# Kernel tuning notes

Hardware: AMD Instinct MI355X
Metric: run time of the kernel (lower is better)

## Reference

```python
import jax, jax.numpy as jnp
import numpy as np

DIM_Q = 512
DIM_K = 512
DIM_V = 512
NUM_HEADS = 8
EPS = 1e-5


def _layer_norm(x, g, b):
    m = jnp.mean(x, axis=-1, keepdims=True)
    v = jnp.mean(jnp.square(x - m), axis=-1, keepdims=True)
    return (x - m) * jax.lax.rsqrt(v + EPS) * g + b


def setup_inputs() -> dict:
    key = jax.random.key(0)
    ks = jax.random.split(key, 12)
    B, Sq, Sk = 32, 512, 512
    s_q = 1.0 / np.sqrt(DIM_Q)
    s_v = 1.0 / np.sqrt(DIM_V)
    return {
        "Q": jax.random.normal(ks[0], (B, Sq, DIM_Q), jnp.float32),
        "K": jax.random.normal(ks[1], (B, Sk, DIM_K), jnp.float32),
        "Wq": jax.random.normal(ks[2], (DIM_Q, DIM_V), jnp.float32) * s_q,
        "bq": jnp.zeros((DIM_V,), jnp.float32),
        "Wk": jax.random.normal(ks[3], (DIM_K, DIM_V), jnp.float32) * s_q,
        "bk": jnp.zeros((DIM_V,), jnp.float32),
        "Wv": jax.random.normal(ks[4], (DIM_K, DIM_V), jnp.float32) * s_q,
        "bv": jnp.zeros((DIM_V,), jnp.float32),
        "Wo": jax.random.normal(ks[5], (DIM_V, DIM_V), jnp.float32) * s_v,
        "bo": jnp.zeros((DIM_V,), jnp.float32),
        "ln0_g": jnp.ones((DIM_V,), jnp.float32),
        "ln0_b": jnp.zeros((DIM_V,), jnp.float32),
        "ln1_g": jnp.ones((DIM_V,), jnp.float32),
        "ln1_b": jnp.zeros((DIM_V,), jnp.float32),
    }


def reference(Q, K, Wq, bq, Wk, bk, Wv, bv, Wo, bo, ln0_g, ln0_b, ln1_g, ln1_b):
    B, Sq, _ = Q.shape
    Sk = K.shape[1]
    H = NUM_HEADS
    dh = DIM_V // H
    q = Q @ Wq + bq  # [B, Sq, V]
    k = K @ Wk + bk  # [B, Sk, V]
    v = K @ Wv + bv  # [B, Sk, V]
    # split(dim_split, 2) + cat(dim 0) == standard head split
    qh = q.reshape(B, Sq, H, dh)
    kh = k.reshape(B, Sk, H, dh)
    vh = v.reshape(B, Sk, H, dh)
    # NOTE: original scales by sqrt(dim_V), not sqrt(head_dim)
    scores = jnp.einsum("bqhd,bkhd->bhqk", qh, kh) / np.sqrt(DIM_V)
    A = jax.nn.softmax(scores, axis=-1)  # [B, H, Sq, Sk]
    oh = qh + jnp.einsum("bhqk,bkhd->bqhd", A, vh)  # residual inside heads
    O = oh.reshape(B, Sq, DIM_V)  # cat heads back along feature dim
    O = _layer_norm(O, ln0_g, ln0_b)
    O = O + jax.nn.relu(O @ Wo + bo)
    O = _layer_norm(O, ln1_g, ln1_b)
    return O
```

## Files before the change

kernel.cpp:

```cpp
#include <hip/hip_runtime.h>

#define NB 32
#define SEQ 512
#define DIM 512
#define NH 8
#define DH 64
#define MTOT (NB*SEQ)

typedef __attribute__((ext_vector_type(8))) __bf16 bf16x8;
typedef __attribute__((ext_vector_type(8))) short s16x8;
typedef __attribute__((ext_vector_type(4))) float f32x4;
typedef __attribute__((ext_vector_type(16))) float f32x16;
typedef __attribute__((ext_vector_type(4))) unsigned u32x4;

__device__ __forceinline__ float bf2f(short u) {
    union { float f; unsigned u; } x; x.u = ((unsigned)(unsigned short)u) << 16; return x.f;
}
__device__ __forceinline__ short f2bf(float f) {
    union { float f; unsigned u; } x; x.f = f;
    unsigned r = x.u + 0x7FFFu + ((x.u >> 16) & 1u);
    return (short)(r >> 16);
}

#define MFMA16(a,b,c) __builtin_amdgcn_mfma_f32_16x16x32_bf16(a,b,c,0,0,0)
#define MFMA32(a,b,c) __builtin_amdgcn_mfma_f32_32x32x16_bf16(a,b,c,0,0,0)

__device__ __forceinline__ void gload_lds16(const void* g, void* l) {
    __builtin_amdgcn_global_load_lds(
        (const __attribute__((address_space(1))) unsigned int*)g,
        (__attribute__((address_space(3))) unsigned int*)l, 16, 0, 0);
}
__device__ __forceinline__ unsigned cvt_pk_bf16(float lo, float hi) {
    unsigned r;
    asm("v_cvt_pk_bf16_f32 %0, %1, %2" : "=v"(r) : "v"(lo), "v"(hi));
    return r;
}

__global__ __launch_bounds__(256) void k_wprep(
    const float* __restrict__ Wq, const float* __restrict__ Wk,
    const float* __restrict__ Wv, const float* __restrict__ Wo,
    short* __restrict__ Wt)
{
    __shared__ float t[64][65];
    const float* W = blockIdx.z==0?Wq: blockIdx.z==1?Wk: blockIdx.z==2?Wv:Wo;
    short* out = Wt + (size_t)blockIdx.z*DIM*DIM;
    int k0 = blockIdx.x*64, n0 = blockIdx.y*64;
    int c = threadIdx.x & 63, r4 = threadIdx.x >> 6;
    #pragma unroll
    for (int i=0;i<16;i++){ int r = i*4 + r4; t[r][c] = W[(size_t)(k0+r)*DIM + n0 + c]; }
    __syncthreads();
    #pragma unroll
    for (int i=0;i<16;i++){ int r = i*4 + r4; out[(size_t)(n0+r)*DIM + k0 + c] = f2bf(t[c][r]); }
}

__global__ __launch_bounds__(256) void k_projqkv(
    const float* __restrict__ Q, const float* __restrict__ K,
    const short* __restrict__ Wt,
    const float* __restrict__ bq, const float* __restrict__ bk, const float* __restrict__ bv,
    short* __restrict__ qb, short* __restrict__ kb, short* __restrict__ vT)
{
    __shared__ __align__(16) char pool[49152];
    short* lds = (short*)pool;
    const int tid = threadIdx.x;
    const int wave = tid >> 6, lane = tid & 63;
    const int z = blockIdx.z;
    const float* A   = (z==0) ? Q : K;
    const short* W   = Wt + z*(DIM*DIM);
    const float* bia = (z==0)?bq:(z==1)?bk:bv;
    const int m0 = blockIdx.x*128, n0 = blockIdx.y*128;

    const float* srcA[4];
    #pragma unroll
    for (int i=0;i<4;i++) {
        int P = i*256 + tid, r = P>>3, pc = P&7, lc = pc ^ (r&7);
        srcA[i] = A + (size_t)(m0+r)*DIM + lc*4;
    }
    const short* srcB[2];
    #pragma unroll
    for (int i=0;i<2;i++) {
        int P = i*256 + tid, r = P>>2, c = P&3;
        srcB[i] = W + (size_t)(n0+r)*DIM + ((c ^ ((r>>1)&3))<<3);
    }

#define PSTAGE(T, BUF) do { \
        const int k0_ = (T)*32; \
        char* dA_ = pool + (BUF)*16384; \
        char* dB_ = pool + 32768 + (BUF)*8192; \
        gload_lds16(srcA[0] + k0_, dA_ +         wave*1024); \
        gload_lds16(srcA[1] + k0_, dA_ +  4096 + wave*1024); \
        gload_lds16(srcA[2] + k0_, dA_ +  8192 + wave*1024); \
        gload_lds16(srcA[3] + k0_, dA_ + 12288 + wave*1024); \
        gload_lds16(srcB[0] + k0_, dB_ +         wave*1024); \
        gload_lds16(srcB[1] + k0_, dB_ +  4096 + wave*1024); \
    } while(0)

    const int wr = (wave>>1)*64, wc = (wave&1)*64;
    const int fr = lane & 15, kg = lane >> 4;

    f32x4 acc[4][4];
    #pragma unroll
    for (int i=0;i<4;i++)
        #pragma unroll
        for (int j=0;j<4;j++) acc[i][j] = (f32x4){0.f,0.f,0.f,0.f};

    PSTAGE(0, 0);
    PSTAGE(1, 1);

    for (int t=0; t<16; ++t) {
        const int cur = t & 1;
        if (t < 15) asm volatile("s_waitcnt vmcnt(6)" ::: "memory");
        else        asm volatile("s_waitcnt vmcnt(0)" ::: "memory");
        asm volatile("s_barrier" ::: "memory");

        const char* pA = pool + cur*16384;
        const char* pB = pool + 32768 + cur*8192;
        float4 alo[4], ahi[4];
        #pragma unroll
        for (int f=0; f<4; ++f) {
            int R = wr + f*16 + fr;
            const char* base = pA + R*128;
            alo[f] = *(const float4*)(base + ((((kg<<1)  ) ^ (R&7))<<4));
            ahi[f] = *(const float4*)(base + ((((kg<<1)|1) ^ (R&7))<<4));
        }
        bf16x8 bfr[4];
        #pragma unroll
        for (int f=0; f<4; ++f) {
            int Rb = wc + f*16 + fr;
            bfr[f] = *(const bf16x8*)(pB + Rb*64 + ((kg ^ ((Rb>>1)&3))<<4));
        }
        asm volatile("s_waitcnt lgkmcnt(0)" ::: "memory");
        asm volatile("s_barrier" ::: "memory");
        if (t < 14) PSTAGE(t+2, cur);

        bf16x8 af[4];
        #pragma unroll
        for (int f=0; f<4; ++f) {
            u32x4 pk = { cvt_pk_bf16(alo[f].x, alo[f].y), cvt_pk_bf16(alo[f].z, alo[f].w),
                         cvt_pk_bf16(ahi[f].x, ahi[f].y), cvt_pk_bf16(ahi[f].z, ahi[f].w) };
            af[f] = __builtin_bit_cast(bf16x8, pk);
        }
        #pragma unroll
        for (int i=0;i<4;i++)
            #pragma unroll
            for (int j=0;j<4;j++) acc[i][j] = MFMA16(af[i], bfr[j], acc[i][j]);
    }
#undef PSTAGE
    __syncthreads();

    const int r0 = (lane>>4)*4;
    #pragma unroll
    for (int i=0;i<4;i++)
        #pragma unroll
        for (int j=0;j<4;j++) {
            int row = wr + i*16 + r0;
            int col = wc + j*16 + fr;
            float bb = bia[n0 + col];
            #pragma unroll
            for (int r=0;r<4;r++) lds[(row+r)*136 + col] = f2bf(acc[i][j][r] + bb);
        }
    __syncthreads();
    if (z < 2) {
        short* out = (z==0)? qb : kb;
        int row = tid>>1, ch = (tid&1)*64;
        #pragma unroll
        for (int j=0;j<8;j++) {
            int col = ch + j*8;
            s16x8 v = *(s16x8*)&lds[row*136 + col];
            *(s16x8*)&out[(size_t)(m0+row)*DIM + n0 + col] = v;
        }
    } else {
        int c = tid>>1, sh = (tid&1)*64;
        int b = m0 >> 9;
        int h = (n0 + c) >> 6, d = (n0 + c) & 63;
        size_t base = ((size_t)(b*NH + h)*DH + d)*SEQ + (m0 & 511) + sh;
        #pragma unroll
        for (int i8=0;i8<8;i8++) {
            s16x8 tv;
            #pragma unroll
            for (int j=0;j<8;j++) tv[j] = lds[(sh + i8*8 + j)*136 + c];
            *(s16x8*)&vT[base + i8*8] = tv;
        }
    }
}

__global__ __launch_bounds__(256, 2) void k_attn(
    const short* __restrict__ qb, const short* __restrict__ kb,
    const short* __restrict__ vT, short* __restrict__ Oh)
{
    __shared__ short pool[9216];
    __shared__ float invLds[4][2][32];
    char* poolB = (char*)pool;
    const int tid = threadIdx.x, wave = tid>>6, lane = tid&63;
    const int l31 = lane & 31, hi = lane >> 5;
    const int b = blockIdx.z, h = blockIdx.y;
    const int bh = b*NH + h;
    const int bx = blockIdx.x;
    const float SCALE = 0.0441941738241592f;

    bf16x8 qf[2][4];
    #pragma unroll
    for (int u=0; u<2; ++u)
        #pragma unroll
        for (int d=0; d<4; ++d)
            qf[u][d] = *(const bf16x8*)&qb[(size_t)(b*SEQ + bx*256 + u*128 + wave*32 + l31)*DIM + h*DH + d*16 + hi*8];

    const short* gK0 = kb + (size_t)(b*SEQ + l31)*DIM + h*DH + wave*16 + hi*8;
    const short* gV0 = vT + ((size_t)bh*DH + (wave>>1)*32 + l31)*SEQ + (wave&1)*16 + hi*8;

    f32x16 o[2][2];
    #pragma unroll
    for (int u=0;u<2;u++)
        #pragma unroll
        for (int q=0;q<2;q++)
            #pragma unroll
            for (int r=0;r<16;r++) o[u][q][r]=0.f;
    float lsum[2] = {0.f, 0.f};

    gload_lds16(gK0,            poolB + wave*1024);
    gload_lds16(gV0,            poolB + 8192 + wave*1024);

    for (int kt=0; kt<16; ++kt) {
        const int p = kt & 1;
        __syncthreads();
        if (kt < 15) {
            gload_lds16(gK0 + (size_t)(kt+1)*32*DIM, poolB + (p^1)*4096 + wave*1024);
            gload_lds16(gV0 + (kt+1)*32,             poolB + 8192 + (p^1)*4096 + wave*1024);
        }
        const char* Kb = poolB + p*4096 + lane*16;
        bf16x8 kf0 = *(const bf16x8*)(Kb);
        bf16x8 kf1 = *(const bf16x8*)(Kb + 1024);
        bf16x8 kf2 = *(const bf16x8*)(Kb + 2048);
        bf16x8 kf3 = *(const bf16x8*)(Kb + 3072);
        const char* Vb = poolB + 8192 + p*4096 + lane*16;
        bf16x8 v00 = *(const bf16x8*)(Vb);
        bf16x8 v01 = *(const bf16x8*)(Vb + 1024);
        bf16x8 v10 = *(const bf16x8*)(Vb + 2048);
        bf16x8 v11 = *(const bf16x8*)(Vb + 3072);
        #pragma unroll
        for (int u=0; u<2; ++u) {
            f32x16 s;
            #pragma unroll
            for (int r=0;r<16;r++) s[r]=0.f;
            s = MFMA32(kf0, qf[u][0], s);
            s = MFMA32(kf1, qf[u][1], s);
            s = MFMA32(kf2, qf[u][2], s);
            s = MFMA32(kf3, qf[u][3], s);
            float pe[16];
            #pragma unroll
            for (int r=0;r<16;r++) { pe[r] = __expf(s[r]*SCALE - 3.0f); lsum[u] += pe[r]; }
            unsigned pk0 = cvt_pk_bf16(pe[0],  pe[1]);
            unsigned pk1 = cvt_pk_bf16(pe[2],  pe[3]);
            unsigned pk2 = cvt_pk_bf16(pe[4],  pe[5]);
            unsigned pk3 = cvt_pk_bf16(pe[6],  pe[7]);
            unsigned pk4 = cvt_pk_bf16(pe[8],  pe[9]);
            unsigned pk5 = cvt_pk_bf16(pe[10], pe[11]);
            unsigned pk6 = cvt_pk_bf16(pe[12], pe[13]);
            unsigned pk7 = cvt_pk_bf16(pe[14], pe[15]);
            asm("v_permlane32_swap_b32 %0, %1" : "+v"(pk0), "+v"(pk2));
            asm("v_permlane32_swap_b32 %0, %1" : "+v"(pk1), "+v"(pk3));
            asm("v_permlane32_swap_b32 %0, %1" : "+v"(pk4), "+v"(pk6));
            asm("v_permlane32_swap_b32 %0, %1" : "+v"(pk5), "+v"(pk7));
            u32x4 f0w = {pk0, pk1, pk2, pk3};
            u32x4 f1w = {pk4, pk5, pk6, pk7};
            bf16x8 F0 = __builtin_bit_cast(bf16x8, f0w);
            bf16x8 F1 = __builtin_bit_cast(bf16x8, f1w);
            o[u][0] = MFMA32(F0, v00, o[u][0]);
            o[u][0] = MFMA32(F1, v01, o[u][0]);
            o[u][1] = MFMA32(F0, v10, o[u][1]);
            o[u][1] = MFMA32(F1, v11, o[u][1]);
        }
    }
    float linv[2];
    #pragma unroll
    for (int u=0;u<2;u++) { float v = lsum[u]; v += __shfl_xor(v, 32); linv[u] = 1.0f / v; }
    __syncthreads();
    if (lane < 32) { invLds[wave][0][l31] = linv[0]; invLds[wave][1][l31] = linv[1]; }
    short* O = pool + wave*2304;
    #pragma unroll
    for (int u=0; u<2; ++u) {
        #pragma unroll
        for (int r=0;r<16;r++) {
            int q = (r&3) + 8*(r>>2) + 4*hi;
            float iq = invLds[wave][u][q];
            O[q*72 + l31]      = f2bf(o[u][0][r] * iq);
            O[q*72 + 32 + l31] = f2bf(o[u][1][r] * iq);
        }
        int rr = lane>>1, c0 = (lane&1)*32;
        size_t baseO = ((size_t)bh*SEQ + bx*256 + u*128 + wave*32 + rr)*DH + c0;
        #pragma unroll
        for (int j=0;j<4;j++) {
            s16x8 v = *(s16x8*)&O[rr*72 + c0 + j*8];
            *(s16x8*)&Oh[baseO + j*8] = v;
        }
    }
}

__global__ __launch_bounds__(256) void k_ln0(
    const short* __restrict__ qb, const short* __restrict__ Oh,
    const float* __restrict__ g, const float* __restrict__ bt,
    short* __restrict__ x0)
{
    int wave = threadIdx.x>>6, lane = threadIdx.x&63;
    int row = blockIdx.x*4 + wave;
    int b = row >> 9, s = row & 511;
    int f0 = lane*8;
    s16x8 qv = *(const s16x8*)&qb[(size_t)row*DIM + f0];
    int h = f0 >> 6, d = f0 & 63;
    s16x8 ov = *(const s16x8*)&Oh[((size_t)(b*NH+h)*SEQ + s)*DH + d];
    float x[8];
    float sm=0.f, sq=0.f;
    #pragma unroll
    for (int j=0;j<8;j++) { x[j] = bf2f(qv[j]) + bf2f(ov[j]); sm += x[j]; sq += x[j]*x[j]; }
    #pragma unroll
    for (int off=1; off<64; off<<=1) { sm += __shfl_xor(sm,off); sq += __shfl_xor(sq,off); }
    float mean = sm*(1.0f/512.0f);
    float var  = sq*(1.0f/512.0f) - mean*mean;
    float inv  = rsqrtf(var + 1e-5f);
    float4 g0 = *(const float4*)&g[f0],  g1 = *(const float4*)&g[f0+4];
    float4 t0 = *(const float4*)&bt[f0], t1 = *(const float4*)&bt[f0+4];
    s16x8 outv;
    outv[0]=f2bf((x[0]-mean)*inv*g0.x + t0.x); outv[1]=f2bf((x[1]-mean)*inv*g0.y + t0.y);
    outv[2]=f2bf((x[2]-mean)*inv*g0.z + t0.z); outv[3]=f2bf((x[3]-mean)*inv*g0.w + t0.w);
    outv[4]=f2bf((x[4]-mean)*inv*g1.x + t1.x); outv[5]=f2bf((x[5]-mean)*inv*g1.y + t1.y);
    outv[6]=f2bf((x[6]-mean)*inv*g1.z + t1.z); outv[7]=f2bf((x[7]-mean)*inv*g1.w + t1.w);
    *(s16x8*)&x0[(size_t)row*DIM + f0] = outv;
}

__global__ __launch_bounds__(512) void k_gemmy_ln(
    const short* __restrict__ x0, const short* __restrict__ Wto,
    const float* __restrict__ bo,
    const float* __restrict__ g, const float* __restrict__ bt,
    float* __restrict__ out)
{
    __shared__ __align__(16) char pool[73728];
    const int tid = threadIdx.x;
    const int wave = tid >> 6, lane = tid & 63;
    const int fr = lane & 15, g4 = lane >> 4;

    int L = ((int)blockIdx.x & 7)*32 + ((int)blockIdx.x >> 3);
    const int m0 = L*64;

    size_t srcA = 0;
    if (wave < 4) {
        int r = tid>>2, c = tid&3;
        srcA = (size_t)(m0 + r)*DIM + ((c ^ ((r>>1)&3))<<3);
    }
    size_t srcB[4];
    #pragma unroll
    for (int i=0;i<4;i++) {
        int s = i*512 + tid, r = s>>2, c = s&3;
        srcB[i] = (size_t)r*DIM + ((c ^ ((r>>1)&3))<<3);
    }

    f32x4 acc[16];
    #pragma unroll
    for (int j=0;j<16;j++) acc[j] = (f32x4){0.f,0.f,0.f,0.f};

#define GSTAGE(T, BUF) do { \
        const short* As_ = x0  + (T)*32; \
        const short* Bs_ = Wto + (T)*32; \
        if (wave < 4) gload_lds16(As_ + srcA, pool + (BUF)*4096 + wave*1024); \
        char* dB_ = pool + 8192 + (BUF)*32768; \
        gload_lds16(Bs_ + srcB[0], dB_ +     0 + wave*1024); \
        gload_lds16(Bs_ + srcB[1], dB_ +  8192 + wave*1024); \
        gload_lds16(Bs_ + srcB[2], dB_ + 16384 + wave*1024); \
        gload_lds16(Bs_ + srcB[3], dB_ + 24576 + wave*1024); \
    } while(0)

    GSTAGE(0, 0);
    __syncthreads();

    int cur = 0;
    for (int t=0; t<16; ++t) {
        if (t < 15) GSTAGE(t+1, cur^1);
        const char* pA = pool + cur*4096;
        const char* pB = pool + 8192 + cur*32768;
        int R = (wave>>1)*16 + fr;
        bf16x8 af = *(const bf16x8*)(pA + R*64 + ((g4 ^ ((R>>1)&3))<<4));
        #pragma unroll
        for (int j=0;j<16;j++) {
            int Rb = (wave&1)*256 + j*16 + fr;
            bf16x8 bf = *(const bf16x8*)(pB + Rb*64 + ((g4 ^ ((Rb>>1)&3))<<4));
            acc[j] = MFMA16(af, bf, acc[j]);
        }
        __syncthreads();
        cur ^= 1;
    }
#undef GSTAGE

    short (*Lo)[520] = (short(*)[520])pool;
    {
        int wrow = (wave>>1)*16 + g4*4;
        int cbase = (wave&1)*256;
        #pragma unroll
        for (int j=0;j<16;j++) {
            int col = cbase + j*16 + fr;
            float bb = bo[col];
            #pragma unroll
            for (int r=0;r<4;r++) {
                float vv = acc[j][r] + bb;
                vv = vv > 0.f ? vv : 0.f;
                Lo[wrow + r][col] = f2bf(vv);
            }
        }
    }
    __syncthreads();

    int f0 = lane*8;
    float4 gg0 = *(const float4*)&g[f0],  gg1 = *(const float4*)&g[f0+4];
    float4 tt0 = *(const float4*)&bt[f0], tt1 = *(const float4*)&bt[f0+4];
    #pragma unroll
    for (int rr=0; rr<8; ++rr) {
        int row = wave*8 + rr;
        s16x8 rv = *(s16x8*)&Lo[row][f0];
        s16x8 xv = *(const s16x8*)&x0[(size_t)(m0+row)*DIM + f0];
        float x[8];
        float sm=0.f, sq=0.f;
        #pragma unroll
        for (int j=0;j<8;j++) { x[j] = bf2f(rv[j]) + bf2f(xv[j]); sm += x[j]; sq += x[j]*x[j]; }
        #pragma unroll
        for (int off=1; off<64; off<<=1) { sm += __shfl_xor(sm,off); sq += __shfl_xor(sq,off); }
        float mean = sm*(1.0f/512.0f);
        float var  = sq*(1.0f/512.0f) - mean*mean;
        float inv  = rsqrtf(var + 1e-5f);
        float4 o0, o1;
        o0.x=(x[0]-mean)*inv*gg0.x + tt0.x; o0.y=(x[1]-mean)*inv*gg0.y + tt0.y;
        o0.z=(x[2]-mean)*inv*gg0.z + tt0.z; o0.w=(x[3]-mean)*inv*gg0.w + tt0.w;
        o1.x=(x[4]-mean)*inv*gg1.x + tt1.x; o1.y=(x[5]-mean)*inv*gg1.y + tt1.y;
        o1.z=(x[6]-mean)*inv*gg1.z + tt1.z; o1.w=(x[7]-mean)*inv*gg1.w + tt1.w;
        *(float4*)&out[(size_t)(m0+row)*DIM + f0]     = o0;
        *(float4*)&out[(size_t)(m0+row)*DIM + f0 + 4] = o1;
    }
}

extern "C" void kernel_launch(void* const* d_in, const int* in_sizes, int n_in,
                              void* d_out, int out_size, void* d_ws, size_t ws_size,
                              hipStream_t stream)
{
    const float* Q  = (const float*)d_in[0];
    const float* K  = (const float*)d_in[1];
    const float* Wq = (const float*)d_in[2];
    const float* bq = (const float*)d_in[3];
    const float* Wk = (const float*)d_in[4];
    const float* bk = (const float*)d_in[5];
    const float* Wv = (const float*)d_in[6];
    const float* bv = (const float*)d_in[7];
    const float* Wo = (const float*)d_in[8];
    const float* bo = (const float*)d_in[9];
    const float* g0 = (const float*)d_in[10];
    const float* be0= (const float*)d_in[11];
    const float* g1 = (const float*)d_in[12];
    const float* be1= (const float*)d_in[13];
    float* out = (float*)d_out;

    char* ws = (char*)d_ws;
    size_t off = 0;
    short* Wt = (short*)(ws + off); off += (size_t)4*DIM*DIM*2;
    short* qb = (short*)(ws + off); off += (size_t)MTOT*DIM*2;
    short* kb = (short*)(ws + off); off += (size_t)MTOT*DIM*2;
    short* vT = (short*)(ws + off); off += (size_t)MTOT*DIM*2;
    short* Oh = (short*)(ws + off); off += (size_t)MTOT*DIM*2;
    short* x0 = vT;

    k_wprep   <<<dim3(8,8,4),   256, 0, stream>>>(Wq,Wk,Wv,Wo,Wt);
    k_projqkv <<<dim3(128,4,3), 256, 0, stream>>>(Q,K,Wt,bq,bk,bv,qb,kb,vT);
    k_attn    <<<dim3(2,NH,NB), 256, 0, stream>>>(qb,kb,vT,Oh);
    k_ln0     <<<dim3(MTOT/4),  256, 0, stream>>>(qb,Oh,g0,be0,x0);
    k_gemmy_ln<<<dim3(256),     512, 0, stream>>>(x0, Wt + (size_t)3*DIM*DIM, bo, g1, be1, out);
}
```

Before: 135.1 us.

## Shrink projection LDS staging and restructure output GEMM wait/barrier pipeline

In the QKV projection kernel, the A tile now uses a single LDS buffer that is reloaded one stage ahead, while B keeps a two-stage double buffer. This cuts shared memory from 48KB to 34KB, which could allow more resident blocks per CU. In the output-projection GEMM, the full __syncthreads is replaced with explicit vmcnt waits and barriers, and all B fragments are loaded into registers before the MFMAs so the next stage's loads overlap compute. The costs are a shallower prefetch for A, higher register pressure from holding 16 B fragments, and hand-tuned vmcnt counts that must exactly match the number of loads issued per wave.

```diff
diff --git a/kernel.cpp b/kernel.cpp
--- a/kernel.cpp
+++ b/kernel.cpp
@@ -59,7 +59,7 @@
     const float* __restrict__ bq, const float* __restrict__ bk, const float* __restrict__ bv,
     short* __restrict__ qb, short* __restrict__ kb, short* __restrict__ vT)
 {
-    __shared__ __align__(16) char pool[49152];
+    __shared__ __align__(16) char pool[34816];
     short* lds = (short*)pool;
     const int tid = threadIdx.x;
     const int wave = tid >> 6, lane = tid & 63;
@@ -82,16 +82,18 @@
         srcB[i] = W + (size_t)(n0+r)*DIM + ((c ^ ((r>>1)&3))<<3);
     }
 
-#define PSTAGE(T, BUF) do { \
+#define ASTAGE(T) do { \
         const int k0_ = (T)*32; \
-        char* dA_ = pool + (BUF)*16384; \
-        char* dB_ = pool + 32768 + (BUF)*8192; \
-        gload_lds16(srcA[0] + k0_, dA_ +         wave*1024); \
-        gload_lds16(srcA[1] + k0_, dA_ +  4096 + wave*1024); \
-        gload_lds16(srcA[2] + k0_, dA_ +  8192 + wave*1024); \
-        gload_lds16(srcA[3] + k0_, dA_ + 12288 + wave*1024); \
-        gload_lds16(srcB[0] + k0_, dB_ +         wave*1024); \
-        gload_lds16(srcB[1] + k0_, dB_ +  4096 + wave*1024); \
+        gload_lds16(srcA[0] + k0_, pool +         wave*1024); \
+        gload_lds16(srcA[1] + k0_, pool +  4096 + wave*1024); \
+        gload_lds16(srcA[2] + k0_, pool +  8192 + wave*1024); \
+        gload_lds16(srcA[3] + k0_, pool + 12288 + wave*1024); \
+    } while(0)
+#define BSTAGE(T) do { \
+        const int k0_ = (T)*32; \
+        char* dB_ = pool + 16384 + ((T)&1)*8192; \
+        gload_lds16(srcB[0] + k0_, dB_ +        wave*1024); \
+        gload_lds16(srcB[1] + k0_, dB_ + 4096 + wave*1024); \
     } while(0)
 
     const int wr = (wave>>1)*64, wc = (wave&1)*64;
@@ -103,25 +105,22 @@
         #pragma unroll
         for (int j=0;j<4;j++) acc[i][j] = (f32x4){0.f,0.f,0.f,0.f};
 
-    PSTAGE(0, 0);
-    PSTAGE(1, 1);
+    ASTAGE(0); BSTAGE(0); BSTAGE(1);
 
     for (int t=0; t<16; ++t) {
-        const int cur = t & 1;
-        if (t < 15) asm volatile("s_waitcnt vmcnt(6)" ::: "memory");
+        if (t < 15) asm volatile("s_waitcnt vmcnt(2)" ::: "memory");
         else        asm volatile("s_waitcnt vmcnt(0)" ::: "memory");
         asm volatile("s_barrier" ::: "memory");
 
-        const char* pA = pool + cur*16384;
-        const char* pB = pool + 32768 + cur*8192;
         float4 alo[4], ahi[4];
         #pragma unroll
         for (int f=0; f<4; ++f) {
             int R = wr + f*16 + fr;
-            const char* base = pA + R*128;
+            const char* base = pool + R*128;
             alo[f] = *(const float4*)(base + ((((kg<<1)  ) ^ (R&7))<<4));
             ahi[f] = *(const float4*)(base + ((((kg<<1)|1) ^ (R&7))<<4));
         }
+        const char* pB = pool + 16384 + (t&1)*8192;
         bf16x8 bfr[4];
         #pragma unroll
         for (int f=0; f<4; ++f) {
@@ -130,7 +129,8 @@
         }
         asm volatile("s_waitcnt lgkmcnt(0)" ::: "memory");
         asm volatile("s_barrier" ::: "memory");
-        if (t < 14) PSTAGE(t+2, cur);
+        if (t < 15) ASTAGE(t+1);
+        if (t < 14) BSTAGE(t+2);
 
         bf16x8 af[4];
         #pragma unroll
@@ -144,7 +144,8 @@
             #pragma unroll
             for (int j=0;j<4;j++) acc[i][j] = MFMA16(af[i], bfr[j], acc[i][j]);
     }
-#undef PSTAGE
+#undef ASTAGE
+#undef BSTAGE
     __syncthreads();
 
     const int r0 = (lane>>4)*4;
@@ -368,22 +369,33 @@
     } while(0)
 
     GSTAGE(0, 0);
-    __syncthreads();
 
     int cur = 0;
     for (int t=0; t<16; ++t) {
         if (t < 15) GSTAGE(t+1, cur^1);
+        if (t == 15) {
+            asm volatile("s_waitcnt vmcnt(0)" ::: "memory");
+        } else if (wave < 4) {
+            asm volatile("s_waitcnt vmcnt(5)" ::: "memory");
+        } else {
+            asm volatile("s_waitcnt vmcnt(4)" ::: "memory");
+        }
+        asm volatile("s_barrier" ::: "memory");
+
         const char* pA = pool + cur*4096;
         const char* pB = pool + 8192 + cur*32768;
         int R = (wave>>1)*16 + fr;
         bf16x8 af = *(const bf16x8*)(pA + R*64 + ((g4 ^ ((R>>1)&3))<<4));
+        bf16x8 bfv[16];
         #pragma unroll
         for (int j=0;j<16;j++) {
             int Rb = (wave&1)*256 + j*16 + fr;
-            bf16x8 bf = *(const bf16x8*)(pB + Rb*64 + ((g4 ^ ((Rb>>1)&3))<<4));
-            acc[j] = MFMA16(af, bf, acc[j]);
-        }
-        __syncthreads();
+            bfv[j] = *(const bf16x8*)(pB + Rb*64 + ((g4 ^ ((Rb>>1)&3))<<4));
+        }
+        asm volatile("s_waitcnt lgkmcnt(0)" ::: "memory");
+        asm volatile("s_barrier" ::: "memory");
+        #pragma unroll
+        for (int j=0;j<16;j++) acc[j] = MFMA16(af, bfv[j], acc[j]);
         cur ^= 1;
     }
 #undef GSTAGE
```

After: 135.5 us. Within noise of the previous version (+0.3%).

## Enlarge QKV projection tiles to 256x256 with 512 threads and interleaved MFMA

Applied to the files above, without the earlier changes.

The QKV projection GEMM moves from 128x128 tiles with 4 waves to 256x256 tiles with 8 waves, each wave computing a 128x64 sub-tile. The aim is more reuse of each staged A and B tile and fewer global loads per output. The K-loop now interleaves A-fragment LDS reads and bf16 conversion with MFMA groups under s_setprio, and the epilogue writes the output through LDS in two halves. The trade-offs are 96KB of LDS per block, doubled accumulator registers, and a grid of only 384 blocks, which can hurt occupancy and load balance across CUs.

```diff
diff --git a/kernel.cpp b/kernel.cpp
--- a/kernel.cpp
+++ b/kernel.cpp
@@ -53,132 +53,141 @@
     for (int i=0;i<16;i++){ int r = i*4 + r4; out[(size_t)(n0+r)*DIM + k0 + c] = f2bf(t[c][r]); }
 }
 
-__global__ __launch_bounds__(256) void k_projqkv(
+__global__ __launch_bounds__(512) void k_projqkv(
     const float* __restrict__ Q, const float* __restrict__ K,
     const short* __restrict__ Wt,
     const float* __restrict__ bq, const float* __restrict__ bk, const float* __restrict__ bv,
     short* __restrict__ qb, short* __restrict__ kb, short* __restrict__ vT)
 {
-    __shared__ __align__(16) char pool[49152];
-    short* lds = (short*)pool;
+    __shared__ __align__(16) char pool[98304];
     const int tid = threadIdx.x;
     const int wave = tid >> 6, lane = tid & 63;
     const int z = blockIdx.z;
     const float* A   = (z==0) ? Q : K;
     const short* W   = Wt + z*(DIM*DIM);
     const float* bia = (z==0)?bq:(z==1)?bk:bv;
-    const int m0 = blockIdx.x*128, n0 = blockIdx.y*128;
+    const int m0 = blockIdx.x*256, n0 = blockIdx.y*256;
 
     const float* srcA[4];
     #pragma unroll
     for (int i=0;i<4;i++) {
-        int P = i*256 + tid, r = P>>3, pc = P&7, lc = pc ^ (r&7);
-        srcA[i] = A + (size_t)(m0+r)*DIM + lc*4;
+        int P = i*512 + tid, r = P>>3, c = P&7;
+        srcA[i] = A + (size_t)(m0+r)*DIM + ((c ^ (r&7))<<2);
     }
     const short* srcB[2];
     #pragma unroll
     for (int i=0;i<2;i++) {
-        int P = i*256 + tid, r = P>>2, c = P&3;
+        int P = i*512 + tid, r = P>>2, c = P&3;
         srcB[i] = W + (size_t)(n0+r)*DIM + ((c ^ ((r>>1)&3))<<3);
     }
 
-#define PSTAGE(T, BUF) do { \
+#define STAGE(T) do { \
         const int k0_ = (T)*32; \
-        char* dA_ = pool + (BUF)*16384; \
-        char* dB_ = pool + 32768 + (BUF)*8192; \
+        char* dA_ = pool + ((T)&1)*32768; \
+        char* dB_ = pool + 65536 + ((T)&1)*16384; \
         gload_lds16(srcA[0] + k0_, dA_ +         wave*1024); \
-        gload_lds16(srcA[1] + k0_, dA_ +  4096 + wave*1024); \
-        gload_lds16(srcA[2] + k0_, dA_ +  8192 + wave*1024); \
-        gload_lds16(srcA[3] + k0_, dA_ + 12288 + wave*1024); \
+        gload_lds16(srcA[1] + k0_, dA_ +  8192 + wave*1024); \
+        gload_lds16(srcA[2] + k0_, dA_ + 16384 + wave*1024); \
+        gload_lds16(srcA[3] + k0_, dA_ + 24576 + wave*1024); \
         gload_lds16(srcB[0] + k0_, dB_ +         wave*1024); \
-        gload_lds16(srcB[1] + k0_, dB_ +  4096 + wave*1024); \
+        gload_lds16(srcB[1] + k0_, dB_ +  8192 + wave*1024); \
     } while(0)
 
-    const int wr = (wave>>1)*64, wc = (wave&1)*64;
+    const int wr = (wave>>2)*128, wc = (wave&3)*64;
     const int fr = lane & 15, kg = lane >> 4;
 
-    f32x4 acc[4][4];
-    #pragma unroll
-    for (int i=0;i<4;i++)
+    f32x4 acc[8][4];
+    #pragma unroll
+    for (int i=0;i<8;i++)
         #pragma unroll
         for (int j=0;j<4;j++) acc[i][j] = (f32x4){0.f,0.f,0.f,0.f};
 
-    PSTAGE(0, 0);
-    PSTAGE(1, 1);
+    STAGE(0); STAGE(1);
+    asm volatile("s_waitcnt vmcnt(6)" ::: "memory");
+    asm volatile("s_barrier" ::: "memory");
 
     for (int t=0; t<16; ++t) {
-        const int cur = t & 1;
-        if (t < 15) asm volatile("s_waitcnt vmcnt(6)" ::: "memory");
-        else        asm volatile("s_waitcnt vmcnt(0)" ::: "memory");
-        asm volatile("s_barrier" ::: "memory");
-
-        const char* pA = pool + cur*16384;
-        const char* pB = pool + 32768 + cur*8192;
-        float4 alo[4], ahi[4];
-        #pragma unroll
-        for (int f=0; f<4; ++f) {
-            int R = wr + f*16 + fr;
-            const char* base = pA + R*128;
-            alo[f] = *(const float4*)(base + ((((kg<<1)  ) ^ (R&7))<<4));
-            ahi[f] = *(const float4*)(base + ((((kg<<1)|1) ^ (R&7))<<4));
-        }
+        const char* pA = pool + (t&1)*32768;
+        const char* pB = pool + 65536 + (t&1)*16384;
+
         bf16x8 bfr[4];
         #pragma unroll
-        for (int f=0; f<4; ++f) {
-            int Rb = wc + f*16 + fr;
-            bfr[f] = *(const bf16x8*)(pB + Rb*64 + ((kg ^ ((Rb>>1)&3))<<4));
-        }
+        for (int j=0;j<4;j++) {
+            int Rb = wc + j*16 + fr;
+            bfr[j] = *(const bf16x8*)(pB + Rb*64 + ((kg ^ ((Rb>>1)&3))<<4));
+        }
+        #pragma unroll
+        for (int p=0;p<4;p++) {
+            bf16x8 af[2];
+            #pragma unroll
+            for (int q=0;q<2;q++) {
+                int f = p*2 + q;
+                int R = wr + f*16 + fr;
+                const char* base = pA + R*128;
+                float4 lo = *(const float4*)(base + ((((kg<<1)  ) ^ (R&7))<<4));
+                float4 hi = *(const float4*)(base + ((((kg<<1)|1) ^ (R&7))<<4));
+                u32x4 pk = { cvt_pk_bf16(lo.x,lo.y), cvt_pk_bf16(lo.z,lo.w),
+                             cvt_pk_bf16(hi.x,hi.y), cvt_pk_bf16(hi.z,hi.w) };
+                af[q] = __builtin_bit_cast(bf16x8, pk);
+            }
+            __builtin_amdgcn_s_setprio(1);
+            #pragma unroll
+            for (int q=0;q<2;q++)
+                #pragma unroll
+                for (int j=0;j<4;j++) acc[p*2+q][j] = MFMA16(af[q], bfr[j], acc[p*2+q][j]);
+            __builtin_amdgcn_s_setprio(0);
+        }
+
         asm volatile("s_waitcnt lgkmcnt(0)" ::: "memory");
         asm volatile("s_barrier" ::: "memory");
-        if (t < 14) PSTAGE(t+2, cur);
-
-        bf16x8 af[4];
-        #pragma unroll
-        for (int f=0; f<4; ++f) {
-            u32x4 pk = { cvt_pk_bf16(alo[f].x, alo[f].y), cvt_pk_bf16(alo[f].z, alo[f].w),
-                         cvt_pk_bf16(ahi[f].x, ahi[f].y), cvt_pk_bf16(ahi[f].z, ahi[f].w) };
-            af[f] = __builtin_bit_cast(bf16x8, pk);
-        }
-        #pragma unroll
-        for (int i=0;i<4;i++)
-            #pragma unroll
-            for (int j=0;j<4;j++) acc[i][j] = MFMA16(af[i], bfr[j], acc[i][j]);
-    }
-#undef PSTAGE
-    __syncthreads();
-
+        if (t < 14) {
+            STAGE(t+2);
+            asm volatile("s_waitcnt vmcnt(6)" ::: "memory");
+        } else if (t == 14) {
+            asm volatile("s_waitcnt vmcnt(0)" ::: "memory");
+        }
+        asm volatile("s_barrier" ::: "memory");
+    }
+#undef STAGE
+
+    short (*Ov)[264] = (short(*)[264])pool;
     const int r0 = (lane>>4)*4;
     #pragma unroll
-    for (int i=0;i<4;i++)
-        #pragma unroll
-        for (int j=0;j<4;j++) {
-            int row = wr + i*16 + r0;
-            int col = wc + j*16 + fr;
-            float bb = bia[n0 + col];
-            #pragma unroll
-            for (int r=0;r<4;r++) lds[(row+r)*136 + col] = f2bf(acc[i][j][r] + bb);
-        }
-    __syncthreads();
-    if (z < 2) {
-        short* out = (z==0)? qb : kb;
-        int row = tid>>1, ch = (tid&1)*64;
-        #pragma unroll
-        for (int j=0;j<8;j++) {
-            int col = ch + j*8;
-            s16x8 v = *(s16x8*)&lds[row*136 + col];
-            *(s16x8*)&out[(size_t)(m0+row)*DIM + n0 + col] = v;
-        }
-    } else {
-        int c = tid>>1, sh = (tid&1)*64;
-        int b = m0 >> 9;
-        int h = (n0 + c) >> 6, d = (n0 + c) & 63;
-        size_t base = ((size_t)(b*NH + h)*DH + d)*SEQ + (m0 & 511) + sh;
-        #pragma unroll
-        for (int i8=0;i8<8;i8++) {
-            s16x8 tv;
-            #pragma unroll
-            for (int j=0;j<8;j++) tv[j] = lds[(sh + i8*8 + j)*136 + c];
-            *(s16x8*)&vT[base + i8*8] = tv;
+    for (int hh=0; hh<2; ++hh) {
+        __syncthreads();
+        if ((wave>>2) == hh) {
+            #pragma unroll
+            for (int f=0;f<8;f++)
+                #pragma unroll
+                for (int j=0;j<4;j++) {
+                    int row = f*16 + r0;
+                    int col = wc + j*16 + fr;
+                    float bb = bia[n0 + col];
+                    #pragma unroll
+                    for (int r=0;r<4;r++) Ov[row+r][col] = f2bf(acc[f][j][r] + bb);
+                }
+        }
+        __syncthreads();
+        if (z < 2) {
+            short* outp = (z==0)? qb : kb;
+            int row = tid>>2, cs = (tid&3)*64;
+            #pragma unroll
+            for (int j=0;j<8;j++) {
+                s16x8 v = *(s16x8*)&Ov[row][cs + j*8];
+                *(s16x8*)&outp[(size_t)(m0+hh*128+row)*DIM + n0 + cs + j*8] = v;
+            }
+        } else {
+            int c = tid>>1, sh = (tid&1)*64;
+            int b = m0 >> 9;
+            int h = (n0 + c) >> 6, d = (n0 + c) & 63;
+            size_t base = ((size_t)(b*NH + h)*DH + d)*SEQ + (m0 & 511) + hh*128 + sh;
+            #pragma unroll
+            for (int i8=0;i8<8;i8++) {
+                s16x8 tv;
+                #pragma unroll
+                for (int j=0;j<8;j++) tv[j] = Ov[sh + i8*8 + j][c];
+                *(s16x8*)&vT[base + i8*8] = tv;
+            }
         }
     }
 }
@@ -463,7 +472,7 @@
     short* x0 = vT;
 
     k_wprep   <<<dim3(8,8,4),   256, 0, stream>>>(Wq,Wk,Wv,Wo,Wt);
-    k_projqkv <<<dim3(128,4,3), 256, 0, stream>>>(Q,K,Wt,bq,bk,bv,qb,kb,vT);
+    k_projqkv <<<dim3(64,2,3),  512, 0, stream>>>(Q,K,Wt,bq,bk,bv,qb,kb,vT);
     k_attn    <<<dim3(2,NH,NB), 256, 0, stream>>>(qb,kb,vT,Oh);
     k_ln0     <<<dim3(MTOT/4),  256, 0, stream>>>(qb,Oh,g0,be0,x0);
     k_gemmy_ln<<<dim3(256),     512, 0, stream>>>(x0, Wt + (size_t)3*DIM*DIM, bo, g1, be1, out);
```

Result: slower. 148.6 us (+10.0%).
